# Kernel tuning notes

Measured on AMD Instinct MI355X. Metric: run time of the kernel, lower is better.

The kernel has to match this reference:

```python
import jax, jax.numpy as jnp
import numpy as np

EPS = 1e-7

def _masked_stats(x, w, k):
    # Parallel equivalent of the sequential Welford update_counter loop:
    # after the loop, mean = running mean, s = sum of squared deviations (M2),
    # std = sqrt(s / (k - 1)). Computed under no_grad in torch -> stop_gradient.
    m = jnp.sum(x * w, axis=0) / k
    s = jnp.sum(w * (x - m) ** 2, axis=0)
    std = jnp.sqrt(s / (k - 1.0))
    return jax.lax.stop_gradient(m), jax.lax.stop_gradient(std)

def _mlp(x, W1, b1, W2, b2):
    # MlpClass(d, d, 2*d, n_hidden=1) with relu act: d -> 2d -> d
    return jax.nn.relu(x @ W1 + b1) @ W2 + b2

def setup_inputs() -> dict:
    key = jax.random.key(0)
    ks = jax.random.split(key, 8)
    B, S, XD, DD = 8, 2048, 1024, 4096
    scale = 0.02
    return {
        "u": jax.random.normal(ks[0], (B, S, XD), jnp.float32),
        "v": jax.random.normal(ks[1], (B, S, DD), jnp.float32),
        "u_W1": jax.random.normal(ks[2], (XD, 2 * XD), jnp.float32) * scale,
        "u_b1": jnp.zeros((2 * XD,), jnp.float32),
        "u_W2": jax.random.normal(ks[3], (2 * XD, XD), jnp.float32) * scale,
        "u_b2": jnp.zeros((XD,), jnp.float32),
        "v_W1": jax.random.normal(ks[4], (DD, 2 * DD), jnp.float32) * scale,
        "v_b1": jnp.zeros((2 * DD,), jnp.float32),
        "v_W2": jax.random.normal(ks[5], (2 * DD, DD), jnp.float32) * scale,
        "v_b2": jnp.zeros((DD,), jnp.float32),
    }

def reference(u, v, u_W1, u_b1, u_W2, u_b2, v_W1, v_b1, v_W2, v_b2):
    u_ = u.reshape(-1, u.shape[-1]).astype(jnp.float32)  # [N, x_dim]
    v_ = v.reshape(-1, v.shape[-1]).astype(jnp.float32)  # [N, delta_dim]
    # nonzero-row mask; torch drops masked rows, we zero them (equivalent math,
    # static shapes). With randn inputs no row is masked.
    nz = jnp.any(u_ != 0, axis=-1) & jnp.any(v_ != 0, axis=-1)
    w = nz.astype(u_.dtype)[:, None]  # [N, 1]
    k = jnp.sum(w)
    u_mean, u_std = _masked_stats(u_, w, k)
    v_mean, v_std = _masked_stats(v_, w, k)
    u_input = (u_ - u_mean) / (u_std + EPS)
    v_input = (v_ - v_mean) / (v_std + EPS)
    out1 = _mlp(u_input, u_W1, u_b1, u_W2, u_b2) * w
    out2 = _mlp(v_input, v_W1, v_b1, v_W2, v_b2) * w
    return out1, out2
```

## Files before the change

kernel.cpp:

```cpp
#include <hip/hip_runtime.h>
#include <hip/hip_bf16.h>

#define NROWS 16384
#define XD 1024
#define DD 4096

typedef __attribute__((ext_vector_type(8))) short short8;
typedef __attribute__((ext_vector_type(4))) float f32x4;

__device__ __forceinline__ unsigned short f2bf(float f) {
  unsigned int u = __builtin_bit_cast(unsigned int, f);
  u += 0x7fffu + ((u >> 16) & 1u);
  return (unsigned short)(u >> 16);
}

__device__ __forceinline__ void load_lds16(const void* g, void* l) {
  __builtin_amdgcn_global_load_lds((const __attribute__((address_space(1))) void*)g,
                                   (__attribute__((address_space(3))) void*)l, 16, 0, 0);
}

__global__ __launch_bounds__(256) void mask_kernel(const float* __restrict__ u,
                                                   const float* __restrict__ v,
                                                   float* __restrict__ w) {
  int r = blockIdx.x;
  int t = threadIdx.x;
  const f32x4* up = (const f32x4*)(u + (size_t)r * XD);
  const f32x4* vp = (const f32x4*)(v + (size_t)r * DD);
  f32x4 a = up[t];
  int fu = __syncthreads_or((a.x != 0.f) | (a.y != 0.f) | (a.z != 0.f) | (a.w != 0.f));
  int fv = 0;
#pragma unroll
  for (int it = 0; it < DD / (256 * 4); ++it) {
    if (!fv) {
      f32x4 b = vp[it * 256 + t];
      fv = __syncthreads_or((b.x != 0.f) | (b.y != 0.f) | (b.z != 0.f) | (b.w != 0.f));
    }
  }
  if (t == 0) w[r] = (fu && fv) ? 1.f : 0.f;
}

__global__ __launch_bounds__(256) void ksum_kernel(const float* __restrict__ w,
                                                   float* __restrict__ kout) {
  __shared__ float sm[256];
  float s = 0.f;
  for (int i = threadIdx.x; i < NROWS; i += 256) s += w[i];
  sm[threadIdx.x] = s;
  __syncthreads();
  for (int st = 128; st > 0; st >>= 1) {
    if (threadIdx.x < st) sm[threadIdx.x] += sm[threadIdx.x + st];
    __syncthreads();
  }
  if (threadIdx.x == 0) kout[0] = sm[0];
}

__global__ __launch_bounds__(256) void colstats_partial(const float* __restrict__ X, int cols,
                                                        const float* __restrict__ w,
                                                        float* __restrict__ p1,
                                                        float* __restrict__ p2) {
  int c = blockIdx.x * 256 + threadIdx.x;
  int r0 = blockIdx.y * (NROWS / 64);
  float s1 = 0.f, s2 = 0.f;
  for (int r = r0; r < r0 + NROWS / 64; ++r) {
    float wr = w[r];
    float x = X[(size_t)r * cols + c];
    float xw = x * wr;
    s1 += xw;
    s2 += xw * x;
  }
  p1[(size_t)blockIdx.y * cols + c] = s1;
  p2[(size_t)blockIdx.y * cols + c] = s2;
}

__global__ __launch_bounds__(256) void colstats_final(const float* __restrict__ p1,
                                                      const float* __restrict__ p2,
                                                      const float* __restrict__ kptr, int cols,
                                                      float* __restrict__ mean,
                                                      float* __restrict__ inv) {
  int c = blockIdx.x * 256 + threadIdx.x;
  float s1 = 0.f, s2 = 0.f;
  for (int j = 0; j < 64; ++j) {
    s1 += p1[(size_t)j * cols + c];
    s2 += p2[(size_t)j * cols + c];
  }
  float k = kptr[0];
  float m = s1 / k;
  float s = s2 - s1 * s1 / k;
  float sd = sqrtf(fmaxf(s, 0.f) / (k - 1.f));
  mean[c] = m;
  inv[c] = 1.f / (sd + 1e-7f);
}

__global__ __launch_bounds__(256) void wt_kernel(const float* __restrict__ W, int R, int C,
                                                 unsigned short* __restrict__ T) {
  __shared__ unsigned short tile[64][65];
  int r0 = blockIdx.x * 64, c0 = blockIdx.y * 64;
  int tr = threadIdx.x >> 2;
  int tc = (threadIdx.x & 3) * 16;
  const float* src = W + (size_t)(r0 + tr) * C + c0 + tc;
#pragma unroll
  for (int i = 0; i < 16; i += 4) {
    f32x4 v4 = *(const f32x4*)(src + i);
    tile[tr][tc + i + 0] = f2bf(v4.x);
    tile[tr][tc + i + 1] = f2bf(v4.y);
    tile[tr][tc + i + 2] = f2bf(v4.z);
    tile[tr][tc + i + 3] = f2bf(v4.w);
  }
  __syncthreads();
  unsigned short* dst = T + (size_t)(c0 + tr) * R + r0 + tc;
  short8 o0, o1;
#pragma unroll
  for (int i = 0; i < 8; ++i) o0[i] = (short)tile[tc + i][tr];
#pragma unroll
  for (int i = 0; i < 8; ++i) o1[i] = (short)tile[tc + 8 + i][tr];
  *(short8*)(dst) = o0;
  *(short8*)(dst + 8) = o1;
}

__global__ __launch_bounds__(256) void norm_kernel(const float* __restrict__ X,
                                                   const float* __restrict__ mean,
                                                   const float* __restrict__ inv,
                                                   unsigned short* __restrict__ O,
                                                   int colmask, size_t n8) {
  size_t stride = (size_t)gridDim.x * 256;
  for (size_t i = (size_t)blockIdx.x * 256 + threadIdx.x; i < n8; i += stride) {
    int c8 = (int)(i & (size_t)colmask);
    const float* xp = X + i * 8;
    f32x4 a = *(const f32x4*)xp;
    f32x4 b = *(const f32x4*)(xp + 4);
    f32x4 m0 = *(const f32x4*)(mean + c8 * 8);
    f32x4 m1 = *(const f32x4*)(mean + c8 * 8 + 4);
    f32x4 i0 = *(const f32x4*)(inv + c8 * 8);
    f32x4 i1 = *(const f32x4*)(inv + c8 * 8 + 4);
    short8 p;
    p[0] = (short)f2bf((a.x - m0.x) * i0.x);
    p[1] = (short)f2bf((a.y - m0.y) * i0.y);
    p[2] = (short)f2bf((a.z - m0.z) * i0.z);
    p[3] = (short)f2bf((a.w - m0.w) * i0.w);
    p[4] = (short)f2bf((b.x - m1.x) * i1.x);
    p[5] = (short)f2bf((b.y - m1.y) * i1.y);
    p[6] = (short)f2bf((b.z - m1.z) * i1.z);
    p[7] = (short)f2bf((b.w - m1.w) * i1.w);
    *(short8*)(O + i * 8) = p;
  }
}

template <int EPI>
__global__ __launch_bounds__(512, 2) void gemm8p(const unsigned short* __restrict__ A,
                                                 const unsigned short* __restrict__ Bt,
                                                 const float* __restrict__ bias,
                                                 const float* __restrict__ wrow,
                                                 void* __restrict__ OutP,
                                                 int N, int K) {
  __shared__ char lds[131072];
  const int tid = threadIdx.x;
  const int lane = tid & 63;
  const int wave = tid >> 6;
  const int wr = wave >> 2;
  const int wc = wave & 3;

  const int gn = N >> 8;
  const int nwg = gridDim.x;
  const int bid = blockIdx.x;
  const int sw = (nwg & 7) ? bid : ((bid & 7) * (nwg >> 3) + (bid >> 3));
  const int m0 = (sw / gn) << 8;
  const int n0 = (sw % gn) << 8;

  const int srow = lane >> 3;
  const int scol = ((lane & 7) ^ srow) << 3;

  const int NT = K >> 6;
  f32x4 acc[8][4] = {};

  char* const Abase = lds + wr * 16384;
  char* const Bbase = lds + 65536 + (wc >> 1) * 16384;
  const int bcol = (wc & 1) * 64;
  const int fr = lane & 15;
  const int kbyte = (lane >> 4) << 4;

#define STAGE(T, BUF)                                                              \
  {                                                                                \
    const int k0_ = (T) << 6;                                                      \
    _Pragma("unroll") for (int i = 0; i < 4; ++i) {                                \
      const int row_ = i * 64 + wave * 8 + srow;                                   \
      const int co_ = (i * 8 + wave) * 1024;                                       \
      load_lds16(A + (size_t)(m0 + row_) * K + k0_ + scol, lds + (BUF)*32768 + co_); \
      load_lds16(Bt + (size_t)(n0 + row_) * K + k0_ + scol,                        \
                 lds + 65536 + (BUF)*32768 + co_);                                 \
    }                                                                              \
  }

  STAGE(0, 0);
  __syncthreads();

  for (int t = 0; t < NT; ++t) {
    const int buf = t & 1;
    const int ab = buf * 32768;
    if (t + 1 < NT) STAGE(t + 1, buf ^ 1);

    short8 bfr[2][4];
#pragma unroll
    for (int s = 0; s < 2; ++s)
#pragma unroll
      for (int g = 0; g < 4; ++g) {
        const int r = bcol + g * 16 + fr;
        const int kb = s * 64 + kbyte;
        bfr[s][g] = *(const short8*)(Bbase + ab + r * 128 + (kb ^ ((r & 7) << 4)));
      }

    short8 afA[2][2], afB[2][2];
#pragma unroll
    for (int p = 0; p < 2; ++p)
#pragma unroll
      for (int s = 0; s < 2; ++s) {
        const int r = p * 16 + fr;
        const int kb = s * 64 + kbyte;
        afA[p][s] = *(const short8*)(Abase + ab + r * 128 + (kb ^ ((r & 7) << 4)));
      }
#pragma unroll
    for (int q = 0; q < 4; ++q) {
      if (q < 3) {
#pragma unroll
        for (int p = 0; p < 2; ++p)
#pragma unroll
          for (int s = 0; s < 2; ++s) {
            const int r = ((q + 1) * 2 + p) * 16 + fr;
            const int kb = s * 64 + kbyte;
            short8 vf = *(const short8*)(Abase + ab + r * 128 + (kb ^ ((r & 7) << 4)));
            if (q & 1) afA[p][s] = vf; else afB[p][s] = vf;
          }
      }
      __builtin_amdgcn_s_setprio(1);
#pragma unroll
      for (int p = 0; p < 2; ++p)
#pragma unroll
        for (int s = 0; s < 2; ++s)
#pragma unroll
          for (int g = 0; g < 4; ++g) {
            const short8 av = (q & 1) ? afB[p][s] : afA[p][s];
            acc[q * 2 + p][g] =
                __builtin_amdgcn_mfma_f32_16x16x32_bf16(av, bfr[s][g], acc[q * 2 + p][g], 0, 0, 0);
          }
      __builtin_amdgcn_s_setprio(0);
    }
    __syncthreads();
  }

  const int colloc = wc * 64 + fr;
  const int rowb = wr * 128 + ((lane >> 4) << 2);
  if (EPI == 0) {
    unsigned short* H = (unsigned short*)OutP;
#pragma unroll
    for (int f = 0; f < 8; ++f)
#pragma unroll
      for (int g = 0; g < 4; ++g) {
        const int c = n0 + colloc + g * 16;
        const float b = bias[c];
#pragma unroll
        for (int r = 0; r < 4; ++r) {
          const int row = m0 + rowb + f * 16 + r;
          H[(size_t)row * N + c] = f2bf(fmaxf(acc[f][g][r] + b, 0.f));
        }
      }
  } else {
    float* O = (float*)OutP;
#pragma unroll
    for (int f = 0; f < 8; ++f)
#pragma unroll
      for (int g = 0; g < 4; ++g) {
        const int c = n0 + colloc + g * 16;
        const float b = bias[c];
#pragma unroll
        for (int r = 0; r < 4; ++r) {
          const int row = m0 + rowb + f * 16 + r;
          O[(size_t)row * N + c] = (acc[f][g][r] + b) * wrow[row];
        }
      }
  }
#undef STAGE
}

extern "C" void kernel_launch(void* const* d_in, const int* in_sizes, int n_in,
                              void* d_out, int out_size, void* d_ws, size_t ws_size,
                              hipStream_t stream) {
  const float* u    = (const float*)d_in[0];
  const float* v    = (const float*)d_in[1];
  const float* u_W1 = (const float*)d_in[2];
  const float* u_b1 = (const float*)d_in[3];
  const float* u_W2 = (const float*)d_in[4];
  const float* u_b2 = (const float*)d_in[5];
  const float* v_W1 = (const float*)d_in[6];
  const float* v_b1 = (const float*)d_in[7];
  const float* v_W2 = (const float*)d_in[8];
  const float* v_b2 = (const float*)d_in[9];
  float* out1 = (float*)d_out;
  float* out2 = out1 + (size_t)NROWS * XD;

  float* wsf = (float*)d_ws;
  size_t off = 0;
  float* w_     = wsf + off; off += NROWS;
  float* kv     = wsf + off; off += 16;
  float* u_mean = wsf + off; off += XD;
  float* u_inv  = wsf + off; off += XD;
  float* v_mean = wsf + off; off += DD;
  float* v_inv  = wsf + off; off += DD;
  float* p1u    = wsf + off; off += 64 * XD;
  float* p2u    = wsf + off; off += 64 * XD;
  float* p1v    = wsf + off; off += 64 * DD;
  float* p2v    = wsf + off; off += 64 * DD;

  size_t boff = (off * 4 + 255) & ~(size_t)255;
  unsigned short* W1Tu = (unsigned short*)((char*)d_ws + boff); boff += (size_t)(2 * XD) * XD * 2;
  unsigned short* W2Tu = (unsigned short*)((char*)d_ws + boff); boff += (size_t)XD * (2 * XD) * 2;
  unsigned short* W1Tv = (unsigned short*)((char*)d_ws + boff); boff += (size_t)(2 * DD) * DD * 2;
  unsigned short* W2Tv = (unsigned short*)((char*)d_ws + boff); boff += (size_t)DD * (2 * DD) * 2;
  size_t fixedB = (boff + 255) & ~(size_t)255;

  static const int chs[7] = {16384, 8192, 4096, 2048, 1024, 512, 256};
  int CHu = 256, CHv = 256;
  double best = 1e30;
  for (int a = 0; a < 7; ++a)
    for (int b = 0; b < 7; ++b) {
      int cu = chs[a], cv = chs[b];
      size_t need = fixedB + (size_t)cu * XD * 6 + (size_t)cv * DD * 6 + 1024;
      if (need > ws_size) continue;
      auto util = [](int nwg) { return nwg >= 256 ? 1.0 : nwg / 256.0; };
      double cost = 68.75 / util((cu >> 8) * 8) + 68.75 / util((cu >> 8) * 4) +
                    550.0 / util((cv >> 8) * 32) + 550.0 / util((cv >> 8) * 16);
      if (cost < best) { best = cost; CHu = cu; CHv = cv; }
    }

  size_t p = fixedB;
  unsigned short* unc  = (unsigned short*)((char*)d_ws + p); p += (size_t)CHu * XD * 2;
  unsigned short* uhid = (unsigned short*)((char*)d_ws + p); p += (size_t)CHu * (2 * XD) * 2;
  unsigned short* vnc  = (unsigned short*)((char*)d_ws + p); p += (size_t)CHv * DD * 2;
  unsigned short* vhid = (unsigned short*)((char*)d_ws + p);

  mask_kernel<<<NROWS, 256, 0, stream>>>(u, v, w_);
  ksum_kernel<<<1, 256, 0, stream>>>(w_, kv);
  colstats_partial<<<dim3(XD / 256, 64), 256, 0, stream>>>(u, XD, w_, p1u, p2u);
  colstats_partial<<<dim3(DD / 256, 64), 256, 0, stream>>>(v, DD, w_, p1v, p2v);
  colstats_final<<<XD / 256, 256, 0, stream>>>(p1u, p2u, kv, XD, u_mean, u_inv);
  colstats_final<<<DD / 256, 256, 0, stream>>>(p1v, p2v, kv, DD, v_mean, v_inv);

  wt_kernel<<<dim3(XD / 64, (2 * XD) / 64), 256, 0, stream>>>(u_W1, XD, 2 * XD, W1Tu);
  wt_kernel<<<dim3((2 * XD) / 64, XD / 64), 256, 0, stream>>>(u_W2, 2 * XD, XD, W2Tu);
  wt_kernel<<<dim3(DD / 64, (2 * DD) / 64), 256, 0, stream>>>(v_W1, DD, 2 * DD, W1Tv);
  wt_kernel<<<dim3((2 * DD) / 64, DD / 64), 256, 0, stream>>>(v_W2, 2 * DD, DD, W2Tv);

  for (int r0 = 0; r0 < NROWS; r0 += CHu) {
    size_t n8 = (size_t)CHu * XD / 8;
    int ng = (int)(n8 / 256 < 2048 ? n8 / 256 : 2048);
    norm_kernel<<<ng, 256, 0, stream>>>(u + (size_t)r0 * XD, u_mean, u_inv, unc, XD / 8 - 1, n8);
    gemm8p<0><<<(CHu >> 8) * ((2 * XD) >> 8), 512, 0, stream>>>(unc, W1Tu, u_b1, nullptr, uhid,
                                                                2 * XD, XD);
    gemm8p<1><<<(CHu >> 8) * (XD >> 8), 512, 0, stream>>>(uhid, W2Tu, u_b2, w_ + r0,
                                                          out1 + (size_t)r0 * XD, XD, 2 * XD);
  }
  for (int r0 = 0; r0 < NROWS; r0 += CHv) {
    size_t n8 = (size_t)CHv * DD / 8;
    int ng = (int)(n8 / 256 < 2048 ? n8 / 256 : 2048);
    norm_kernel<<<ng, 256, 0, stream>>>(v + (size_t)r0 * DD, v_mean, v_inv, vnc, DD / 8 - 1, n8);
    gemm8p<0><<<(CHv >> 8) * ((2 * DD) >> 8), 512, 0, stream>>>(vnc, W1Tv, v_b1, nullptr, vhid,
                                                                2 * DD, DD);
    gemm8p<1><<<(CHv >> 8) * (DD >> 8), 512, 0, stream>>>(vhid, W2Tv, v_b2, w_ + r0,
                                                          out2 + (size_t)r0 * DD, DD, 2 * DD);
  }
}
```

Measured before the change: 2.373 ms.

## Restructure GEMM main loop into 4-stage K=32 LDS pipeline with split barriers

The bf16 MFMA GEMM main loop now uses K-steps of 32 instead of 64. Global-to-LDS loads rotate through a 4-buffer ring with three stages prefetched ahead, and explicit vmcnt waits replace the double buffer that synced once per iteration. Each iteration is split into two half-phases. Each half loads fragments, issues a prefetch group and runs 16 MFMAs between s_barriers, with setprio around the compute. The LDS swizzle and fragment layout are also changed. The goal is deeper overlap of memory latency with compute, at the cost of more barriers per K and tricky waitcnt bookkeeping at the loop tail.

```diff
diff --git a/kernel.cpp b/kernel.cpp
--- a/kernel.cpp
+++ b/kernel.cpp
@@ -165,85 +165,82 @@
   const int m0 = (sw / gn) << 8;
   const int n0 = (sw % gn) << 8;
 
-  const int srow = lane >> 3;
-  const int scol = ((lane & 7) ^ srow) << 3;
-
-  const int NT = K >> 6;
+  const int NT = K >> 5;
+
+  const int rl = 2 * (lane >> 3) + ((lane >> 2) & 1);
+  const int sl = (lane & 3) ^ ((lane >> 3) & 3);
+
+  const int fr = lane & 15;
+  const int frag_off =
+      (fr >> 1) * 128 + (fr & 1) * 64 + (((lane >> 4) ^ ((fr >> 1) & 3)) << 4);
+
+#define STAGE_G(T, G)                                                               \
+  {                                                                                 \
+    const int k0_ = (T) << 5;                                                       \
+    const int r_ = (G) * 128 + wave * 16 + rl;                                      \
+    const int co_ = ((G) * 512 + wave * 64) * 16;                                   \
+    const int bo_ = ((T) & 3) * 16384;                                              \
+    load_lds16(A + (size_t)(m0 + r_) * K + k0_ + sl * 8, lds + bo_ + co_);          \
+    load_lds16(Bt + (size_t)(n0 + r_) * K + k0_ + sl * 8, lds + 65536 + bo_ + co_); \
+  }
+
   f32x4 acc[8][4] = {};
 
-  char* const Abase = lds + wr * 16384;
-  char* const Bbase = lds + 65536 + (wc >> 1) * 16384;
-  const int bcol = (wc & 1) * 64;
-  const int fr = lane & 15;
-  const int kbyte = (lane >> 4) << 4;
-
-#define STAGE(T, BUF)                                                              \
-  {                                                                                \
-    const int k0_ = (T) << 6;                                                      \
-    _Pragma("unroll") for (int i = 0; i < 4; ++i) {                                \
-      const int row_ = i * 64 + wave * 8 + srow;                                   \
-      const int co_ = (i * 8 + wave) * 1024;                                       \
-      load_lds16(A + (size_t)(m0 + row_) * K + k0_ + scol, lds + (BUF)*32768 + co_); \
-      load_lds16(Bt + (size_t)(n0 + row_) * K + k0_ + scol,                        \
-                 lds + 65536 + (BUF)*32768 + co_);                                 \
-    }                                                                              \
-  }
-
-  STAGE(0, 0);
-  __syncthreads();
-
+  STAGE_G(0, 0); STAGE_G(0, 1);
+  STAGE_G(1, 0); STAGE_G(1, 1);
+  STAGE_G(2, 0); STAGE_G(2, 1);
+  asm volatile("s_waitcnt vmcnt(8)" ::: "memory");
+  __builtin_amdgcn_sched_barrier(0);
+  __builtin_amdgcn_s_barrier();
+
+  short8 afr[4], bfr[4];
   for (int t = 0; t < NT; ++t) {
-    const int buf = t & 1;
-    const int ab = buf * 32768;
-    if (t + 1 < NT) STAGE(t + 1, buf ^ 1);
-
-    short8 bfr[2][4];
-#pragma unroll
-    for (int s = 0; s < 2; ++s)
-#pragma unroll
-      for (int g = 0; g < 4; ++g) {
-        const int r = bcol + g * 16 + fr;
-        const int kb = s * 64 + kbyte;
-        bfr[s][g] = *(const short8*)(Bbase + ab + r * 128 + (kb ^ ((r & 7) << 4)));
-      }
-
-    short8 afA[2][2], afB[2][2];
-#pragma unroll
-    for (int p = 0; p < 2; ++p)
-#pragma unroll
-      for (int s = 0; s < 2; ++s) {
-        const int r = p * 16 + fr;
-        const int kb = s * 64 + kbyte;
-        afA[p][s] = *(const short8*)(Abase + ab + r * 128 + (kb ^ ((r & 7) << 4)));
-      }
-#pragma unroll
-    for (int q = 0; q < 4; ++q) {
-      if (q < 3) {
-#pragma unroll
-        for (int p = 0; p < 2; ++p)
-#pragma unroll
-          for (int s = 0; s < 2; ++s) {
-            const int r = ((q + 1) * 2 + p) * 16 + fr;
-            const int kb = s * 64 + kbyte;
-            short8 vf = *(const short8*)(Abase + ab + r * 128 + (kb ^ ((r & 7) << 4)));
-            if (q & 1) afA[p][s] = vf; else afB[p][s] = vf;
-          }
-      }
-      __builtin_amdgcn_s_setprio(1);
-#pragma unroll
-      for (int p = 0; p < 2; ++p)
-#pragma unroll
-        for (int s = 0; s < 2; ++s)
-#pragma unroll
-          for (int g = 0; g < 4; ++g) {
-            const short8 av = (q & 1) ? afB[p][s] : afA[p][s];
-            acc[q * 2 + p][g] =
-                __builtin_amdgcn_mfma_f32_16x16x32_bf16(av, bfr[s][g], acc[q * 2 + p][g], 0, 0, 0);
-          }
-      __builtin_amdgcn_s_setprio(0);
+    const int bo = (t & 3) * 16384;
+    const char* Abase = lds + bo + wr * 8192;
+    const char* Bbase = lds + 65536 + bo + wc * 4096;
+
+#pragma unroll
+    for (int g = 0; g < 4; ++g) bfr[g] = *(const short8*)(Bbase + g * 1024 + frag_off);
+#pragma unroll
+    for (int f = 0; f < 4; ++f) afr[f] = *(const short8*)(Abase + f * 1024 + frag_off);
+    if (t + 3 < NT) STAGE_G(t + 3, 0);
+    __builtin_amdgcn_s_barrier();
+    asm volatile("s_waitcnt lgkmcnt(0)" ::: "memory");
+    __builtin_amdgcn_sched_barrier(0);
+    __builtin_amdgcn_s_setprio(1);
+#pragma unroll
+    for (int f = 0; f < 4; ++f)
+#pragma unroll
+      for (int g = 0; g < 4; ++g)
+        acc[f][g] = __builtin_amdgcn_mfma_f32_16x16x32_bf16(afr[f], bfr[g], acc[f][g], 0, 0, 0);
+    __builtin_amdgcn_s_setprio(0);
+    __builtin_amdgcn_s_barrier();
+
+#pragma unroll
+    for (int f = 0; f < 4; ++f) afr[f] = *(const short8*)(Abase + (4 + f) * 1024 + frag_off);
+    if (t + 3 < NT) {
+      STAGE_G(t + 3, 1);
+      asm volatile("s_waitcnt vmcnt(8)" ::: "memory");
+    } else if (t == NT - 3) {
+      asm volatile("s_waitcnt vmcnt(4)" ::: "memory");
+    } else if (t == NT - 2) {
+      asm volatile("s_waitcnt vmcnt(0)" ::: "memory");
     }
-    __syncthreads();
-  }
+    __builtin_amdgcn_sched_barrier(0);
+    __builtin_amdgcn_s_barrier();
+    asm volatile("s_waitcnt lgkmcnt(0)" ::: "memory");
+    __builtin_amdgcn_sched_barrier(0);
+    __builtin_amdgcn_s_setprio(1);
+#pragma unroll
+    for (int f = 0; f < 4; ++f)
+#pragma unroll
+      for (int g = 0; g < 4; ++g)
+        acc[4 + f][g] =
+            __builtin_amdgcn_mfma_f32_16x16x32_bf16(afr[f], bfr[g], acc[4 + f][g], 0, 0, 0);
+    __builtin_amdgcn_s_setprio(0);
+    __builtin_amdgcn_s_barrier();
+  }
+#undef STAGE_G
 
   const int colloc = wc * 64 + fr;
   const int rowb = wr * 128 + ((lane >> 4) << 2);
@@ -276,7 +273,6 @@
         }
       }
   }
-#undef STAGE
 }
 
 extern "C" void kernel_launch(void* const* d_in, const int* in_sizes, int n_in,
```

Measured after the change: 2.596 ms. 1.09x slower.
